# Performance work log

Measured on AMD Instinct MI355X. Metric: run time of the kernel, lower is better.

## Reference

```python
import jax, jax.numpy as jnp
import numpy as np

B, D, H = 4096, 64, 1024  # batch, state dim, hidden width


def setup_inputs() -> dict:
    key = jax.random.key(0)
    ks = jax.random.split(key, 4)
    def w(k, shape, fan_in):
        return (jax.random.normal(k, shape, jnp.float32) / np.float32(np.sqrt(fan_in)))
    return {
        "x": jax.random.normal(ks[0], (B, 1 + D), jnp.float32),
        "W1": w(ks[1], (D, H), D),
        "b1": jnp.zeros((H,), jnp.float32),
        "W2": w(ks[2], (H, H), H),
        "b2": jnp.zeros((H,), jnp.float32),
        "W3": w(ks[3], (H, D), H),
        "b3": jnp.zeros((D,), jnp.float32),
    }


def _mlp(z, W1, b1, W2, b2, W3, b3):
    # tanh MLP vector field: d -> h -> h -> d
    h = jnp.tanh(z @ W1 + b1)
    h = jnp.tanh(h @ W2 + b2)
    return h @ W3 + b3


def reference(x, W1, b1, W2, b2, W3, b3):
    x_in = x[:, 1:]                        # [B, D] state (col 0 is logp channel)
    f = lambda z: _mlp(z, W1, b1, W2, b2, W3, b3)
    x_out = f(x_in)                        # [B, D]

    # Exact Jacobian trace: same math as the torch per-dim autograd.grad loop,
    # expressed as D forward-mode JVPs vmapped over the identity basis.
    eye = jnp.eye(x_in.shape[1], dtype=x.dtype)

    def diag_entry(e):                     # e: [D] basis vector
        _, t = jax.jvp(f, (x_in,), (jnp.broadcast_to(e, x_in.shape),))
        return t @ e                       # [B] = J[:, i, i]

    trJ = jnp.sum(jax.vmap(diag_entry)(eye), axis=0)  # [B]

    out = jnp.concatenate([-trJ[:, None], x_out], axis=1)  # [B, 1+D]
    return out + 0.0 * x  # faithful to `+ 0 * x` in the original
```

## Files before the change

kernel.cpp:

```cpp
#include <hip/hip_runtime.h>
#include <cmath>

typedef unsigned short u16;
typedef __attribute__((ext_vector_type(8))) short s8v;
typedef __attribute__((ext_vector_type(4))) float f4v;
typedef __attribute__((ext_vector_type(16))) float f16v;

__device__ __forceinline__ u16 f2bf(float f) {
    union { float f; unsigned u; } v; v.f = f;
    unsigned r = v.u + 0x7FFFu + ((v.u >> 16) & 1u);
    return (u16)(r >> 16);
}
__device__ __forceinline__ float tanh_fast(float x) {
    float e = __builtin_amdgcn_exp2f(x * 2.88539008177792681f);
    return 1.f - 2.f * __builtin_amdgcn_rcpf(1.f + e);
}
__device__ __forceinline__ int wslot(int row, int c) {
    return ((((c >> 2) << 6) | ((c & 3) << 4) | (row & 15)) ^ c);
}
__device__ __forceinline__ size_t fragoff(int n, int k) {
    return (((size_t)(n >> 5) * 64 + (k >> 4)) * 64 + (n & 31) + (((k >> 3) & 1) << 5)) * 8 + (k & 7);
}

__launch_bounds__(256)
__global__ void cnf_prep(const float* __restrict__ x, const float* __restrict__ W1,
                         const float* __restrict__ W2, const float* __restrict__ W3,
                         u16* __restrict__ W2Tf, u16* __restrict__ VTf,
                         u16* __restrict__ xb, u16* __restrict__ W1T,
                         u16* __restrict__ W3Tf, float* __restrict__ trJ)
{
    __shared__ float w2s[32][33];
    __shared__ __align__(16) float w1s[64][36];
    const int a = blockIdx.x * 32;
    const int b = blockIdx.y * 32;
    const int t = threadIdx.x;

    #pragma unroll
    for (int it = 0; it < 4; ++it) {
        int idx = t + it * 256;
        w2s[idx >> 5][idx & 31] = W2[(a + (idx >> 5)) * 1024 + b + (idx & 31)];
    }
    #pragma unroll
    for (int it = 0; it < 8; ++it) {
        int idx = t + it * 256;
        w1s[idx >> 5][idx & 31] = W1[(idx >> 5) * 1024 + a + (idx & 31)];
    }
    __syncthreads();

    #pragma unroll
    for (int it = 0; it < 4; ++it) {
        int idx = t + it * 256;
        int rr = idx >> 5, cc = idx & 31;
        W2Tf[fragoff(b + rr, a + cc)] = f2bf(w2s[cc][rr]);
    }
    {
        const int q = t >> 3, pg = t & 7;
        const float* w3row = W3 + (b + q) * 64;
        f4v u = f4v{0.f, 0.f, 0.f, 0.f};
        #pragma unroll
        for (int i4 = 0; i4 < 16; ++i4) {
            f4v w3v = *(const f4v*)&w3row[i4 * 4];
            #pragma unroll
            for (int s = 0; s < 4; ++s) {
                f4v wv = *(const f4v*)&w1s[i4 * 4 + s][pg * 4];
                u += w3v[s] * wv;
            }
        }
        #pragma unroll
        for (int j = 0; j < 4; ++j) {
            const int pp = pg * 4 + j;
            VTf[fragoff(b + q, a + pp)] = f2bf(w2s[pp][q] * u[j]);
        }
    }
    {
        int bid = blockIdx.y * 32 + blockIdx.x;
        int e = bid * 256 + t;
        xb[e] = f2bf(x[(e >> 6) * 65 + 1 + (e & 63)]);
    }
    if (blockIdx.y == 0) {
        int pp = t >> 3, i0 = (t & 7) * 8;
        s8v v;
        #pragma unroll
        for (int j = 0; j < 8; ++j) v[j] = (short)f2bf(w1s[i0 + j][pp]);
        *(s8v*)&W1T[(a + pp) * 64 + i0] = v;
        if (t < 128) trJ[blockIdx.x * 128 + t] = 0.f;
    }
    if (blockIdx.y == 1) {
        int idx = blockIdx.x * 256 + t;
        int n = idx & 63, k0 = (idx >> 6) * 8;
        s8v v;
        #pragma unroll
        for (int j = 0; j < 8; ++j) v[j] = (short)f2bf(W3[(k0 + j) * 64 + n]);
        *(s8v*)&W3Tf[fragoff(n, k0)] = v;
    }
}

__launch_bounds__(256)
__global__ void cnf_gemm1(const u16* __restrict__ xb, const u16* __restrict__ W1T,
                          const float* __restrict__ b1,
                          u16* __restrict__ h1, u16* __restrict__ g1)
{
    __shared__ __align__(16) u16 lds[12 * 1024];
    __shared__ __align__(16) u16 hls[128 * 64];
    __shared__ __align__(16) u16 gls[128 * 64];
    const int t = threadIdx.x;
    const int wave = t >> 6, lane = t & 63;
    const int wm = wave >> 1, wn = wave & 1;
    const int g = lane >> 4, lr = lane & 15;
    const int arow0 = blockIdx.x * 128, bcol0 = blockIdx.y * 64;

    #pragma unroll
    for (int i = 0; i < 4; ++i) {
        int ch = t + i * 256, row = ch >> 3, c = ch & 7;
        *(s8v*)&lds[(row >> 4) * 1024 + wslot(row, c) * 8] =
            *(const s8v*)&xb[(arow0 + row) * 64 + c * 8];
    }
    #pragma unroll
    for (int i = 0; i < 2; ++i) {
        int ch = t + i * 256, row = ch >> 3, c = ch & 7;
        *(s8v*)&lds[(8 + (row >> 4)) * 1024 + wslot(row, c) * 8] =
            *(const s8v*)&W1T[(bcol0 + row) * 64 + c * 8];
    }
    __syncthreads();

    f4v acc[4][2];
    #pragma unroll
    for (int mi = 0; mi < 4; ++mi)
        #pragma unroll
        for (int ni = 0; ni < 2; ++ni) acc[mi][ni] = f4v{0.f,0.f,0.f,0.f};

    #pragma unroll
    for (int ks = 0; ks < 2; ++ks) {
        const int lo = (ks * 64 + (lane ^ ((ks * 4 + g) & 7))) * 8;
        s8v af[4], bf[2];
        #pragma unroll
        for (int mi = 0; mi < 4; ++mi) af[mi] = *(const s8v*)&lds[(wm * 4 + mi) * 1024 + lo];
        #pragma unroll
        for (int ni = 0; ni < 2; ++ni) bf[ni] = *(const s8v*)&lds[(8 + wn * 2 + ni) * 1024 + lo];
        #pragma unroll
        for (int mi = 0; mi < 4; ++mi)
            #pragma unroll
            for (int ni = 0; ni < 2; ++ni)
                acc[mi][ni] = __builtin_amdgcn_mfma_f32_16x16x32_bf16(af[mi], bf[ni], acc[mi][ni], 0, 0, 0);
    }

    #pragma unroll
    for (int mi = 0; mi < 4; ++mi) {
        const int rowl = wm * 64 + mi * 16 + g * 4;
        #pragma unroll
        for (int ni = 0; ni < 2; ++ni) {
            const int coll = wn * 32 + ni * 16 + lr;
            const float bv = b1[bcol0 + coll];
            const int cc = coll >> 3, jj = coll & 7;
            #pragma unroll
            for (int r = 0; r < 4; ++r) {
                const int row = rowl + r;
                float h = tanh_fast(acc[mi][ni][r] + bv);
                int idx = row * 64 + ((cc ^ (row & 7)) << 3) + jj;
                hls[idx] = f2bf(h);
                gls[idx] = f2bf(1.f - h * h);
            }
        }
    }
    __syncthreads();

    #pragma unroll
    for (int i = 0; i < 4; ++i) {
        int id = i * 256 + t;
        int row = id >> 3, ch = id & 7;
        int src = row * 64 + ((ch ^ (row & 7)) << 3);
        size_t dst = (size_t)(arow0 + row) * 1024 + bcol0 + ch * 8;
        *(s8v*)&h1[dst] = *(const s8v*)&hls[src];
        *(s8v*)&g1[dst] = *(const s8v*)&gls[src];
    }
}

#define LOADA(dh, dg, ko) \
    do { dh = *(const s8v*)(h1p + (ko)); dg = *(const s8v*)(g1p + (ko)); } while (0)

#define LOADB(B, kkg)                                                          \
    do { _Pragma("unroll")                                                     \
         for (int _ks = 0; _ks < 2; ++_ks) {                                   \
             size_t _o = (((size_t)(ntb + wn) * 64 + (kkg) * 2 + _ks) * 64 + lane) * 8; \
             B[_ks*2 + 0] = *(const s8v*)&W2Tf[_o];                            \
             B[_ks*2 + 1] = *(const s8v*)&VTf[_o];                             \
         } } while (0)

#define WRITEA(sh, sg, bb)                                                     \
    do { u16* _wb = &lds[bb][0];                                               \
         *(s8v*)&_wb[sdst] = sh; *(s8v*)&_wb[4096 + sdst] = sg; } while (0)

#define MIDBODY(kt, AwH, AwG, AlH, AlG, Bc, Bn)                                \
    {                                                                          \
        const u16* buf = &lds[(kt) & 1][0];                                    \
        s8v a1[2][2], a2[2][2];                                                \
        _Pragma("unroll")                                                      \
        for (int ks = 0; ks < 2; ++ks) {                                       \
            const int lp = (lane ^ ((lane >> 5) << 2) ^ (ks << 1)) * 8;        \
            _Pragma("unroll")                                                  \
            for (int mt = 0; mt < 2; ++mt) {                                   \
                const int R = (wrt * 2 + mt) * 2 + ks;                         \
                a1[ks][mt] = *(const s8v*)&buf[R * 512 + lp];                  \
                a2[ks][mt] = *(const s8v*)&buf[4096 + R * 512 + lp];           \
            }                                                                  \
        }                                                                      \
        if ((kt) < 30) { const int _ko = ((kt) + 2) * 32; LOADA(AlH, AlG, _ko); } \
        if ((kt) < 31) { WRITEA(AwH, AwG, ((kt) + 1) & 1); LOADB(Bn, (kt) + 1); } \
        _Pragma("unroll")                                                      \
        for (int ks = 0; ks < 2; ++ks)                                         \
            _Pragma("unroll")                                                  \
            for (int mt = 0; mt < 2; ++mt) {                                   \
                acc1[mt] = __builtin_amdgcn_mfma_f32_32x32x16_bf16(a1[ks][mt], Bc[ks*2+0], acc1[mt], 0, 0, 0); \
                acc2[mt] = __builtin_amdgcn_mfma_f32_32x32x16_bf16(a2[ks][mt], Bc[ks*2+1], acc2[mt], 0, 0, 0); \
            }                                                                  \
        __syncthreads();                                                       \
    }

__launch_bounds__(512, 1)
__global__ void cnf_mid(const u16* __restrict__ h1, const u16* __restrict__ g1,
                        const u16* __restrict__ W2Tf, const u16* __restrict__ VTf,
                        const float* __restrict__ b2,
                        u16* __restrict__ h2f, float* __restrict__ trJ)
{
    __shared__ __align__(16) u16 lds[2][8192];

    const int t = threadIdx.x;
    const int wave = t >> 6, lane = t & 63;
    const int wrt = wave & 1;
    const int wn  = wave >> 1;
    const int bid = blockIdx.x;
    const int bx  = bid >> 3;
    const int by  = bid & 7;
    const int arow0 = bx * 128;
    const int ntb = by * 4;

    const int row = t >> 2, c = t & 3;
    const int R0 = (row >> 5) * 2 + (c >> 1);
    const int L0 = (row & 31) + ((c & 1) << 5);
    const int sdst = (R0 * 64 + (L0 ^ ((L0 >> 5) << 2) ^ ((R0 & 1) << 1))) * 8;
    const u16* h1p = h1 + (size_t)(arow0 + row) * 1024 + c * 8;
    const u16* g1p = g1 + (size_t)(arow0 + row) * 1024 + c * 8;

    f16v acc1[2], acc2[2];
    #pragma unroll
    for (int mt = 0; mt < 2; ++mt)
        #pragma unroll
        for (int r = 0; r < 16; ++r) { acc1[mt][r] = 0.f; acc2[mt][r] = 0.f; }

    s8v ahA, agA, ahB, agB;
    s8v bA[4], bB[4];

    LOADA(ahA, agA, 0);
    WRITEA(ahA, agA, 0);
    LOADA(ahB, agB, 32);
    LOADB(bA, 0);
    __syncthreads();

    for (int kt2 = 0; kt2 < 16; ++kt2) {
        const int kt = kt2 * 2;
        MIDBODY(kt,     ahB, agB, ahA, agA, bA, bB);
        MIDBODY(kt + 1, ahA, agA, ahB, agB, bB, bA);
    }

    const int l31 = lane & 31, lh = lane >> 5;
    #pragma unroll
    for (int mt = 0; mt < 2; ++mt) {
        const int rt = (arow0 >> 5) + wrt * 2 + mt;
        const int q0 = (ntb + wn) * 32;
        const float bv = b2[q0 + l31];
        const size_t hb = (((size_t)rt * 64 + ((q0 + l31) >> 4)) * 64
                           + (((l31 >> 3) & 1) << 5)) * 8 + (l31 & 7) + lh * 32;
        float tr[16];
        #pragma unroll
        for (int r = 0; r < 16; ++r) {
            float hh = tanh_fast(acc1[mt][r] + bv);
            float gg = 1.f - hh * hh;
            h2f[hb + ((r & 3) + ((r >> 2) << 3)) * 8] = f2bf(hh);
            tr[r] = acc2[mt][r] * gg;
        }
        #pragma unroll
        for (int off = 1; off < 32; off <<= 1)
            #pragma unroll
            for (int r = 0; r < 16; ++r) tr[r] += __shfl_xor(tr[r], off);
        if (l31 == 0) {
            const int rowb = arow0 + (wrt * 2 + mt) * 32 + lh * 4;
            #pragma unroll
            for (int r = 0; r < 16; ++r)
                atomicAdd(&trJ[rowb + (r & 3) + ((r >> 2) << 3)], tr[r]);
        }
    }
}

__launch_bounds__(256)
__global__ void cnf_out(const u16* __restrict__ h2f, const u16* __restrict__ W3Tf,
                        const float* __restrict__ b3, const float* __restrict__ trJ,
                        float* __restrict__ out)
{
    __shared__ float red[4][32][32];
    const int t = threadIdx.x;
    const int wave = t >> 6, lane = t & 63;
    const int rt = blockIdx.x;
    const int nb = blockIdx.y;

    f16v acc;
    #pragma unroll
    for (int r = 0; r < 16; ++r) acc[r] = 0.f;

    #pragma unroll
    for (int kki = 0; kki < 16; ++kki) {
        const int kk = wave * 16 + kki;
        s8v af = *(const s8v*)&h2f[(((size_t)rt * 64 + kk) * 64 + lane) * 8];
        s8v bf = *(const s8v*)&W3Tf[(((size_t)nb * 64 + kk) * 64 + lane) * 8];
        acc = __builtin_amdgcn_mfma_f32_32x32x16_bf16(af, bf, acc, 0, 0, 0);
    }
    const int l31 = lane & 31, lh = lane >> 5;
    #pragma unroll
    for (int r = 0; r < 16; ++r)
        red[wave][(r & 3) + ((r >> 2) << 3) + lh * 4][l31] = acc[r];
    __syncthreads();

    #pragma unroll
    for (int i = 0; i < 4; ++i) {
        int o = t + i * 256;
        int row = o >> 5, col = o & 31;
        float s = red[0][row][col] + red[1][row][col] + red[2][row][col]
                + red[3][row][col] + b3[nb * 32 + col];
        out[(size_t)(rt * 32 + row) * 65 + 1 + nb * 32 + col] = s;
    }
    if (nb == 0 && t < 32) out[(size_t)(rt * 32 + t) * 65] = -trJ[rt * 32 + t];
}

extern "C" void kernel_launch(void* const* d_in, const int* in_sizes, int n_in,
                              void* d_out, int out_size, void* d_ws, size_t ws_size,
                              hipStream_t stream) {
    const float* x  = (const float*)d_in[0];
    const float* W1 = (const float*)d_in[1];
    const float* b1 = (const float*)d_in[2];
    const float* W2 = (const float*)d_in[3];
    const float* b2 = (const float*)d_in[4];
    const float* W3 = (const float*)d_in[5];
    const float* b3 = (const float*)d_in[6];
    float* out = (float*)d_out;

    char* ws = (char*)d_ws;
    u16*   h1b = (u16*)(ws);
    u16*   g1b = (u16*)(ws + (size_t)( 8u << 20));
    u16*   h2f = (u16*)(ws + (size_t)(16u << 20));
    u16*   W2T = (u16*)(ws + (size_t)(24u << 20));
    u16*   VTb = (u16*)(ws + (size_t)(26u << 20));
    float* trJ = (float*)(ws + (size_t)(28u << 20));
    u16*   xbb = (u16*)(ws + (size_t)(28u << 20) + 65536);
    u16*   W1T = (u16*)(ws + (size_t)(28u << 20) + 65536 + 524288);
    u16*   W3T = (u16*)(ws + (size_t)(28u << 20) + 65536 + 524288 + 131072);

    cnf_prep <<<dim3(32, 32), 256, 0, stream>>>(x, W1, W2, W3, W2T, VTb, xbb, W1T, W3T, trJ);
    cnf_gemm1<<<dim3(32, 16), 256, 0, stream>>>(xbb, W1T, b1, h1b, g1b);
    cnf_mid  <<<256,          512, 0, stream>>>(h1b, g1b, W2T, VTb, b2, h2f, trJ);
    cnf_out  <<<dim3(128, 2), 256, 0, stream>>>(h2f, W3T, b3, trJ, out);
}
```

Measured before the change: 58.83 us.

## Store h1/g1 in MFMA fragment layout and stage A tiles via direct global-to-LDS loads

```diff
diff --git a/kernel.cpp b/kernel.cpp
--- a/kernel.cpp
+++ b/kernel.cpp
@@ -20,6 +20,12 @@
 }
 __device__ __forceinline__ size_t fragoff(int n, int k) {
     return (((size_t)(n >> 5) * 64 + (k >> 4)) * 64 + (n & 31) + (((k >> 3) & 1) << 5)) * 8 + (k & 7);
+}
+__device__ __forceinline__ void gload_lds16(const u16* g, u16* l) {
+    __builtin_amdgcn_global_load_lds(
+        (const __attribute__((address_space(1))) void*)g,
+        (__attribute__((address_space(3))) void*)l,
+        16, 0, 0);
 }
 
 __launch_bounds__(256)
@@ -98,7 +104,7 @@
 __launch_bounds__(256)
 __global__ void cnf_gemm1(const u16* __restrict__ xb, const u16* __restrict__ W1T,
                           const float* __restrict__ b1,
-                          u16* __restrict__ h1, u16* __restrict__ g1)
+                          u16* __restrict__ h1f, u16* __restrict__ g1f)
 {
     __shared__ __align__(16) u16 lds[12 * 1024];
     __shared__ __align__(16) u16 hls[128 * 64];
@@ -164,19 +170,28 @@
     }
     __syncthreads();
 
+    const int rt0 = arow0 >> 5, kk0 = bcol0 >> 4;
     #pragma unroll
     for (int i = 0; i < 4; ++i) {
-        int id = i * 256 + t;
-        int row = id >> 3, ch = id & 7;
-        int src = row * 64 + ((ch ^ (row & 7)) << 3);
-        size_t dst = (size_t)(arow0 + row) * 1024 + bcol0 + ch * 8;
-        *(s8v*)&h1[dst] = *(const s8v*)&hls[src];
-        *(s8v*)&g1[dst] = *(const s8v*)&gls[src];
-    }
-}
-
-#define LOADA(dh, dg, ko) \
-    do { dh = *(const s8v*)(h1p + (ko)); dg = *(const s8v*)(g1p + (ko)); } while (0)
+        const int tile = (i * 256 + t) >> 6;
+        const int ln = t & 63;
+        const int rt = tile >> 2, kk = tile & 3;
+        const int row = rt * 32 + (ln & 31);
+        const int kb = kk * 16 + (ln >> 5) * 8;
+        const int src = row * 64 + (((kb >> 3) ^ (row & 7)) << 3);
+        const size_t dst = ((size_t)(rt0 + rt) * 64 + (kk0 + kk)) * 512 + ln * 8;
+        *(s8v*)&h1f[dst] = *(const s8v*)&hls[src];
+        *(s8v*)&g1f[dst] = *(const s8v*)&gls[src];
+    }
+}
+
+#define STAGEA(kt, bb)                                                         \
+    do { const int _kkg = (kt) * 2 + kwh;                                      \
+         gload_lds16(h1f + ((size_t)rtg * 64 + _kkg) * 512 + lane * 8,         \
+                     &lds[bb][wave * 512]);                                    \
+         gload_lds16(g1f + ((size_t)rtg * 64 + _kkg) * 512 + lane * 8,         \
+                     &lds[bb][4096 + wave * 512]);                             \
+    } while (0)
 
 #define LOADB(B, kkg)                                                          \
     do { _Pragma("unroll")                                                     \
@@ -186,38 +201,30 @@
              B[_ks*2 + 1] = *(const s8v*)&VTf[_o];                             \
          } } while (0)
 
-#define WRITEA(sh, sg, bb)                                                     \
-    do { u16* _wb = &lds[bb][0];                                               \
-         *(s8v*)&_wb[sdst] = sh; *(s8v*)&_wb[4096 + sdst] = sg; } while (0)
-
-#define MIDBODY(kt, AwH, AwG, AlH, AlG, Bc, Bn)                                \
+#define MIDBODY(kt, Bc, Bn)                                                    \
     {                                                                          \
+        if ((kt) < 31) { STAGEA((kt) + 1, ((kt) + 1) & 1); LOADB(Bn, (kt) + 1); } \
         const u16* buf = &lds[(kt) & 1][0];                                    \
-        s8v a1[2][2], a2[2][2];                                                \
         _Pragma("unroll")                                                      \
         for (int ks = 0; ks < 2; ++ks) {                                       \
-            const int lp = (lane ^ ((lane >> 5) << 2) ^ (ks << 1)) * 8;        \
+            s8v a1[2], a2[2];                                                  \
             _Pragma("unroll")                                                  \
             for (int mt = 0; mt < 2; ++mt) {                                   \
-                const int R = (wrt * 2 + mt) * 2 + ks;                         \
-                a1[ks][mt] = *(const s8v*)&buf[R * 512 + lp];                  \
-                a2[ks][mt] = *(const s8v*)&buf[4096 + R * 512 + lp];           \
+                const int f = ((wrt * 2 + mt) * 2 + ks) * 512 + lane * 8;      \
+                a1[mt] = *(const s8v*)&buf[f];                                 \
+                a2[mt] = *(const s8v*)&buf[4096 + f];                          \
+            }                                                                  \
+            _Pragma("unroll")                                                  \
+            for (int mt = 0; mt < 2; ++mt) {                                   \
+                acc1[mt] = __builtin_amdgcn_mfma_f32_32x32x16_bf16(a1[mt], Bc[ks*2+0], acc1[mt], 0, 0, 0); \
+                acc2[mt] = __builtin_amdgcn_mfma_f32_32x32x16_bf16(a2[mt], Bc[ks*2+1], acc2[mt], 0, 0, 0); \
             }                                                                  \
         }                                                                      \
-        if ((kt) < 30) { const int _ko = ((kt) + 2) * 32; LOADA(AlH, AlG, _ko); } \
-        if ((kt) < 31) { WRITEA(AwH, AwG, ((kt) + 1) & 1); LOADB(Bn, (kt) + 1); } \
-        _Pragma("unroll")                                                      \
-        for (int ks = 0; ks < 2; ++ks)                                         \
-            _Pragma("unroll")                                                  \
-            for (int mt = 0; mt < 2; ++mt) {                                   \
-                acc1[mt] = __builtin_amdgcn_mfma_f32_32x32x16_bf16(a1[ks][mt], Bc[ks*2+0], acc1[mt], 0, 0, 0); \
-                acc2[mt] = __builtin_amdgcn_mfma_f32_32x32x16_bf16(a2[ks][mt], Bc[ks*2+1], acc2[mt], 0, 0, 0); \
-            }                                                                  \
         __syncthreads();                                                       \
     }
 
 __launch_bounds__(512, 1)
-__global__ void cnf_mid(const u16* __restrict__ h1, const u16* __restrict__ g1,
+__global__ void cnf_mid(const u16* __restrict__ h1f, const u16* __restrict__ g1f,
                         const u16* __restrict__ W2Tf, const u16* __restrict__ VTf,
                         const float* __restrict__ b2,
                         u16* __restrict__ h2f, float* __restrict__ trJ)
@@ -233,13 +240,8 @@
     const int by  = bid & 7;
     const int arow0 = bx * 128;
     const int ntb = by * 4;
-
-    const int row = t >> 2, c = t & 3;
-    const int R0 = (row >> 5) * 2 + (c >> 1);
-    const int L0 = (row & 31) + ((c & 1) << 5);
-    const int sdst = (R0 * 64 + (L0 ^ ((L0 >> 5) << 2) ^ ((R0 & 1) << 1))) * 8;
-    const u16* h1p = h1 + (size_t)(arow0 + row) * 1024 + c * 8;
-    const u16* g1p = g1 + (size_t)(arow0 + row) * 1024 + c * 8;
+    const int rtg = bx * 4 + (wave >> 1);
+    const int kwh = wave & 1;
 
     f16v acc1[2], acc2[2];
     #pragma unroll
@@ -247,19 +249,16 @@
         #pragma unroll
         for (int r = 0; r < 16; ++r) { acc1[mt][r] = 0.f; acc2[mt][r] = 0.f; }
 
-    s8v ahA, agA, ahB, agB;
     s8v bA[4], bB[4];
 
-    LOADA(ahA, agA, 0);
-    WRITEA(ahA, agA, 0);
-    LOADA(ahB, agB, 32);
+    STAGEA(0, 0);
     LOADB(bA, 0);
     __syncthreads();
 
     for (int kt2 = 0; kt2 < 16; ++kt2) {
         const int kt = kt2 * 2;
-        MIDBODY(kt,     ahB, agB, ahA, agA, bA, bB);
-        MIDBODY(kt + 1, ahA, agA, ahB, agB, bB, bA);
+        MIDBODY(kt,     bA, bB);
+        MIDBODY(kt + 1, bB, bA);
     }
 
     const int l31 = lane & 31, lh = lane >> 5;
@@ -343,8 +342,8 @@
     float* out = (float*)d_out;
 
     char* ws = (char*)d_ws;
-    u16*   h1b = (u16*)(ws);
-    u16*   g1b = (u16*)(ws + (size_t)( 8u << 20));
+    u16*   h1f = (u16*)(ws);
+    u16*   g1f = (u16*)(ws + (size_t)( 8u << 20));
     u16*   h2f = (u16*)(ws + (size_t)(16u << 20));
     u16*   W2T = (u16*)(ws + (size_t)(24u << 20));
     u16*   VTb = (u16*)(ws + (size_t)(26u << 20));
@@ -354,7 +353,7 @@
     u16*   W3T = (u16*)(ws + (size_t)(28u << 20) + 65536 + 524288 + 131072);
 
     cnf_prep <<<dim3(32, 32), 256, 0, stream>>>(x, W1, W2, W3, W2T, VTb, xbb, W1T, W3T, trJ);
-    cnf_gemm1<<<dim3(32, 16), 256, 0, stream>>>(xbb, W1T, b1, h1b, g1b);
-    cnf_mid  <<<256,          512, 0, stream>>>(h1b, g1b, W2T, VTb, b2, h2f, trJ);
+    cnf_gemm1<<<dim3(32, 16), 256, 0, stream>>>(xbb, W1T, b1, h1f, g1f);
+    cnf_mid  <<<256,          512, 0, stream>>>(h1f, g1f, W2T, VTb, b2, h2f, trJ);
     cnf_out  <<<dim3(128, 2), 256, 0, stream>>>(h2f, W3T, b3, trJ, out);
 }
```

After: 69.16 us. 17.6% more time.
